# Kernel optimization log

Hardware: AMD Instinct MI355X
Metric: run time of the kernel (lower is better)

Reference implementation:

```python
import jax, jax.numpy as jnp
from jax import lax
import numpy as np

B, L, H, P, M = 8, 4096, 256, 512, 1024  # batch, seq_len, h_dim, ssm state dim (2*h), mlp hidden (4*h)

def _ln(x):
    m = jnp.mean(x, -1, keepdims=True)
    v = jnp.mean((x - m) ** 2, -1, keepdims=True)
    return (x - m) * lax.rsqrt(v + 1e-6)

def _mod(x, shift, scale):
    return x * (1.0 + scale[:, None, :]) + shift[:, None, :]

def _mlp(x, w1, b1, w2, b2):
    h = jax.nn.gelu(x @ w1.T + b1, approximate=False)
    return h @ w2.T + b2

def _s5(u, Lre, Lim, Bre, Bim, Cre, Cim, D, log_step):
    # Diagonal S5 with ZOH discretization and bidirectional parallel associative scan.
    Lam = Lre + 1j * Lim                                     # [P] complex diagonal A
    dt = jnp.exp(log_step)                                   # [P]
    Lbar = jnp.exp(Lam * dt)                                 # [P]
    Bbar = ((Lbar - 1.0) / Lam)[:, None] * (Bre + 1j * Bim)  # [P,H]
    Bu = jnp.einsum('blh,ph->blp', u + 0j, Bbar)             # [B,L,P] complex
    a = jnp.broadcast_to(Lbar, Bu.shape)
    def comb(e1, e2):
        a1, b1 = e1
        a2, b2 = e2
        return a2 * a1, a2 * b1 + b2
    xs_f = lax.associative_scan(comb, (a, Bu), axis=1)[1]
    xs_b = lax.associative_scan(comb, (a, Bu[:, ::-1]), axis=1)[1][:, ::-1]
    xs = jnp.concatenate([xs_f, xs_b], axis=-1)              # [B,L,2P]
    y = 2.0 * jnp.real(jnp.einsum('blp,hp->blh', xs, Cre + 1j * Cim))
    return y + D * u

def setup_inputs() -> dict:
    key = jax.random.key(0)
    kit = iter(jax.random.split(key, 80))
    def nrm(shape, s=1.0):
        return jax.random.normal(next(kit), shape, dtype=jnp.float32) * s
    d = {}
    d['ppg_signal'] = nrm((B, H, L))
    d['x_t'] = nrm((B, H, L))
    d['cond'] = nrm((B, H))
    d['w_ada'] = nrm((12 * H, H), 0.02)
    d['b_ada'] = jnp.zeros((12 * H,), jnp.float32)
    for pfx in ('ppg', 'tgt'):
        d[pfx + '_Lre'] = -0.5 - jax.random.uniform(next(kit), (P,), dtype=jnp.float32)
        d[pfx + '_Lim'] = jnp.pi * jnp.arange(P, dtype=jnp.float32)
        d[pfx + '_Bre'] = nrm((P, H), 1.0 / np.sqrt(H))
        d[pfx + '_Bim'] = nrm((P, H), 1.0 / np.sqrt(H))
        d[pfx + '_Cre'] = nrm((H, 2 * P), 1.0 / np.sqrt(2 * P))
        d[pfx + '_Cim'] = nrm((H, 2 * P), 1.0 / np.sqrt(2 * P))
        d[pfx + '_D'] = nrm((H,))
        d[pfx + '_log_step'] = jnp.log(0.001) + (jnp.log(0.1) - jnp.log(0.001)) * jax.random.uniform(next(kit), (P,), dtype=jnp.float32)
    for pfx in ('pre_ppg', 'mlp_ppg', 'pre_tgt', 'post_tgt', 'mlp_tgt'):
        d[pfx + '_w1'] = nrm((M, H), 0.02)
        d[pfx + '_b1'] = jnp.zeros((M,), jnp.float32)
        d[pfx + '_w2'] = nrm((H, M), 0.02)
        d[pfx + '_b2'] = jnp.zeros((H,), jnp.float32)
    return d

def reference(ppg_signal, x_t, cond, w_ada, b_ada, ppg_Lre, ppg_Lim, ppg_Bre, ppg_Bim, ppg_Cre, ppg_Cim, ppg_D, ppg_log_step, tgt_Lre, tgt_Lim, tgt_Bre, tgt_Bim, tgt_Cre, tgt_Cim, tgt_D, tgt_log_step, pre_ppg_w1, pre_ppg_b1, pre_ppg_w2, pre_ppg_b2, mlp_ppg_w1, mlp_ppg_b1, mlp_ppg_w2, mlp_ppg_b2, pre_tgt_w1, pre_tgt_b1, pre_tgt_w2, pre_tgt_b2, post_tgt_w1, post_tgt_b1, post_tgt_w2, post_tgt_b2, mlp_tgt_w1, mlp_tgt_b1, mlp_tgt_w2, mlp_tgt_b2):
    p = jnp.swapaxes(ppg_signal, 1, 2)  # [B,L,H]
    t = jnp.swapaxes(x_t, 1, 2)         # [B,L,H]
    mods = jnp.split(jax.nn.silu(cond) @ w_ada.T + b_ada, 12, axis=1)
    (sh_sp, sc_sp, g_sp, sh_mp, sc_mp, g_mp, sh_st, sc_st, g_st, sh_mt, sc_mt, g_mt) = mods
    res_p = p
    ppg_cond = g_sp[:, None, :] * _s5(_mod(_ln(p), sh_sp, sc_sp), ppg_Lre, ppg_Lim, ppg_Bre, ppg_Bim, ppg_Cre, ppg_Cim, ppg_D, ppg_log_step)
    p = res_p + ppg_cond
    p = res_p + g_mp[:, None, :] * _mlp(_mod(_ln(p), sh_mp, sc_mp), mlp_ppg_w1, mlp_ppg_b1, mlp_ppg_w2, mlp_ppg_b2)
    res_t = t
    tc = g_st[:, None, :] * _s5(_mod(_ln(t), sh_st, sc_st), tgt_Lre, tgt_Lim, tgt_Bre, tgt_Bim, tgt_Cre, tgt_Cim, tgt_D, tgt_log_step)
    pc = _mlp(ppg_cond, pre_ppg_w1, pre_ppg_b1, pre_ppg_w2, pre_ppg_b2)
    tc = _mlp(tc, pre_tgt_w1, pre_tgt_b1, pre_tgt_w2, pre_tgt_b2) + pc
    tc = _mlp(tc, post_tgt_w1, post_tgt_b1, post_tgt_w2, post_tgt_b2)
    t2 = res_t + tc
    dx = res_t + g_mt[:, None, :] * _mlp(_mod(_ln(t2), sh_mt, sc_mt), mlp_tgt_w1, mlp_tgt_b1, mlp_tgt_w2, mlp_tgt_b2)
    return jnp.swapaxes(p, 1, 2), jnp.swapaxes(dx, 1, 2)
```

## Files before the change

kernel.cpp:

```cpp
#include <hip/hip_runtime.h>
#include <hip/hip_bf16.h>
#include <math.h>

typedef unsigned short u16;
typedef unsigned int   u32;
typedef __bf16 bf16x8 __attribute__((ext_vector_type(8)));
typedef u16    u16x8  __attribute__((ext_vector_type(8)));
typedef float  f32x4  __attribute__((ext_vector_type(4)));

#define B_  8
#define L_  4096
#define H_  256
#define P_  512
#define NC_ 32
#define CH_ 128

__device__ __forceinline__ float bf2f(u16 v) { return __uint_as_float(((u32)v) << 16); }
__device__ __forceinline__ u16 f2bf(float f) {
  u32 u = __float_as_uint(f);
  u32 r = u + 0x7FFFu + ((u >> 16) & 1u);
  return (u16)(r >> 16);
}

__device__ __forceinline__ void gload16(const u16* g, u16* l) {
  __builtin_amdgcn_global_load_lds((const __attribute__((address_space(1))) u32*)g,
                                   (__attribute__((address_space(3))) u32*)l, 16, 0, 0);
}

struct F2B10 { const float* s[10]; };
__global__ __launch_bounds__(256) void k_f2b10(F2B10 a, u16* __restrict__ dst) {
  int g = blockIdx.y;
  int i = (blockIdx.x << 8) + threadIdx.x;
  dst[(size_t)g * 262144 + i] = f2bf(a.s[g][i]);
}

__global__ __launch_bounds__(256) void k_mods(const float* __restrict__ cond,
                                              const float* __restrict__ wada,
                                              const float* __restrict__ bada,
                                              float* __restrict__ mods) {
  __shared__ float s[256];
  int b = blockIdx.y;
  int j = (blockIdx.x << 8) + threadIdx.x;
  float c = cond[b * 256 + threadIdx.x];
  s[threadIdx.x] = c / (1.0f + expf(-c));
  __syncthreads();
  float acc = bada[j];
  const float* wr = wada + (size_t)j * 256;
#pragma unroll 8
  for (int k = 0; k < 256; ++k) acc += s[k] * wr[k];
  mods[b * 3072 + j] = acc;
}

__global__ __launch_bounds__(256) void k_tin2(const float* __restrict__ inP,
                                              const float* __restrict__ inT,
                                              u16* __restrict__ Pt, u16* __restrict__ Tt,
                                              int b0, int nb) {
  __shared__ u16 tile[64][65];
  int z = blockIdx.z;
  int sel = (z >= nb);
  int b = sel ? z - nb : z;
  const float* in = sel ? inT : inP;
  u16* out = sel ? Tt : Pt;
  int l0 = blockIdx.x << 6, h0 = blockIdx.y << 6;
  int tx = threadIdx.x, ty = threadIdx.y;
#pragma unroll
  for (int i = 0; i < 16; ++i) {
    int h = h0 + ty + i * 4;
    tile[ty + i * 4][tx] = f2bf(in[((size_t)(b0 + b) * 256 + h) * 4096 + l0 + tx]);
  }
  __syncthreads();
#pragma unroll
  for (int i = 0; i < 16; ++i) {
    int l = l0 + ty + i * 4;
    out[((size_t)b * 4096 + l) * 256 + h0 + tx] = tile[tx][ty + i * 4];
  }
}
__global__ __launch_bounds__(256) void k_tout(const u16* __restrict__ src, float* __restrict__ dst) {
  __shared__ u16 tile[64][65];
  int b = blockIdx.z, l0 = blockIdx.x << 6, h0 = blockIdx.y << 6;
  int tx = threadIdx.x, ty = threadIdx.y;
#pragma unroll
  for (int i = 0; i < 16; ++i) {
    int l = l0 + ty + i * 4;
    tile[ty + i * 4][tx] = src[((size_t)b * 4096 + l) * 256 + h0 + tx];
  }
  __syncthreads();
#pragma unroll
  for (int i = 0; i < 16; ++i) {
    int h = h0 + ty + i * 4;
    dst[((size_t)b * 256 + h) * 4096 + l0 + tx] = bf2f(tile[tx][ty + i * 4]);
  }
}

__global__ __launch_bounds__(256) void k_lnmod(const u16* __restrict__ X, u16* __restrict__ U,
                                               const float* __restrict__ mods,
                                               int sh_off, int sc_off, int b0) {
  int t = blockIdx.x, tid = threadIdx.x;
  int b = b0 + (t >> 12);
  float x = bf2f(X[(size_t)t * 256 + tid]);
  float s1 = x, s2 = x * x;
#pragma unroll
  for (int off = 32; off; off >>= 1) { s1 += __shfl_xor(s1, off); s2 += __shfl_xor(s2, off); }
  __shared__ float red[8];
  int w = tid >> 6;
  if ((tid & 63) == 0) { red[w * 2] = s1; red[w * 2 + 1] = s2; }
  __syncthreads();
  s1 = red[0] + red[2] + red[4] + red[6];
  s2 = red[1] + red[3] + red[5] + red[7];
  float m = s1 * (1.0f / 256.0f);
  float v = fmaxf(s2 * (1.0f / 256.0f) - m * m, 0.0f);
  float r = rsqrtf(v + 1e-6f);
  float sc = mods[b * 3072 + sc_off + tid];
  float sh = mods[b * 3072 + sh_off + tid];
  U[(size_t)t * 256 + tid] = f2bf((x - m) * r * (1.0f + sc) + sh);
}

__global__ __launch_bounds__(256) void k_wb2(const float* Lre0, const float* Lim0, const float* ls0,
                                             const float* Bre0, const float* Bim0, u16* WB0,
                                             const float* Lre1, const float* Lim1, const float* ls1,
                                             const float* Bre1, const float* Bim1, u16* WB1) {
  int s = blockIdx.y;
  const float* Lre = s ? Lre1 : Lre0;
  const float* Lim = s ? Lim1 : Lim0;
  const float* ls  = s ? ls1  : ls0;
  const float* Bre = s ? Bre1 : Bre0;
  const float* Bim = s ? Bim1 : Bim0;
  u16* WB = s ? WB1 : WB0;
  int p = blockIdx.x, h = threadIdx.x;
  float lre = Lre[p], lim = Lim[p];
  float dt = expf(ls[p]);
  float er = expf(lre * dt), sn, cs;
  sincosf(lim * dt, &sn, &cs);
  float ar = er * cs - 1.0f, ai = er * sn;
  float den = lre * lre + lim * lim;
  float cr = (ar * lre + ai * lim) / den;
  float ci = (ai * lre - ar * lim) / den;
  float br = Bre[p * 256 + h], bi = Bim[p * 256 + h];
  WB[(size_t)(2 * p) * 256 + h]     = f2bf(cr * br - ci * bi);
  WB[(size_t)(2 * p + 1) * 256 + h] = f2bf(cr * bi + ci * br);
}

__global__ __launch_bounds__(256) void k_wc2(const float* Cre0, const float* Cim0, u16* W0,
                                             const float* Cre1, const float* Cim1, u16* W1) {
  int s = blockIdx.y;
  const float* Cre = s ? Cre1 : Cre0;
  const float* Cim = s ? Cim1 : Cim0;
  u16* W = s ? W1 : W0;
  int idx = (blockIdx.x << 8) + threadIdx.x;
  int h = idx >> 11, k = idx & 2047;
  int sc = ((k >> 10) << 9) + ((k & 1023) >> 1);
  float v = (k & 1) ? -2.0f * Cim[h * 1024 + sc] : 2.0f * Cre[h * 1024 + sc];
  W[idx] = f2bf(v);
}

__device__ __forceinline__ float2 lbar_of(const float* Lre, const float* Lim, const float* lstep,
                                          int p, float mul) {
  float dt = expf(lstep[p]) * mul;
  float er = expf(Lre[p] * dt), sn, cs;
  sincosf(Lim[p] * dt, &sn, &cs);
  return make_float2(er * cs, er * sn);
}

__global__ __launch_bounds__(256) void k_scanA2(const float* Lre, const float* Lim, const float* lstep,
                                                const u16* __restrict__ Bu,
                                                float2* __restrict__ car_f, float2* __restrict__ car_b) {
  int g = (blockIdx.x << 8) + threadIdx.x;
  int p = g & 511, rb = (g >> 9) & 31, bl = g >> 14;
  float2 a = lbar_of(Lre, Lim, lstep, p, 1.0f);
  float fr = 0.f, fi = 0.f;
  float br_ = 0.f, bi_ = 0.f;
  float pr = 1.f, pi = 0.f;
  const u32* bup = (const u32*)Bu + (((size_t)((bl << 12) + rb * CH_)) << 9) + p;
#pragma unroll 4
  for (int j = 0; j < CH_; ++j) {
    u32 w = *bup;
    float er = bf2f((u16)(w & 0xFFFF)), ei = bf2f((u16)(w >> 16));
    float nr = a.x * fr - a.y * fi + er;
    float ni = a.x * fi + a.y * fr + ei;
    fr = nr; fi = ni;
    br_ += pr * er - pi * ei;
    bi_ += pr * ei + pi * er;
    float npr = pr * a.x - pi * a.y;
    float npi = pr * a.y + pi * a.x;
    pr = npr; pi = npi;
    bup += 512;
  }
  car_f[g] = make_float2(fr, fi);
  car_b[((size_t)bl << 14) + ((size_t)(31 - rb) << 9) + p] = make_float2(br_, bi_);
}

__global__ __launch_bounds__(256) void k_scanB2(const float* Lre, const float* Lim, const float* lstep,
                                                const float2* __restrict__ car_f,
                                                const float2* __restrict__ car_b,
                                                float2* __restrict__ cin_f, float2* __restrict__ cin_b) {
  int dir = blockIdx.y;
  int g = (blockIdx.x << 8) + threadIdx.x;
  int p = g & 511, bl = g >> 9;
  float2 an = lbar_of(Lre, Lim, lstep, p, (float)CH_);
  const float2* car = dir ? car_b : car_f;
  float2* cin = dir ? cin_b : cin_f;
  float xr = 0.f, xi = 0.f;
  size_t base = (size_t)bl * 16384 + p;
  for (int c = 0; c < NC_; ++c) {
    size_t src = base + (size_t)c * 512;
    size_t dst = dir ? (base + (size_t)(31 - c) * 512) : src;
    cin[dst] = make_float2(xr, xi);
    float2 E = car[src];
    float nr = an.x * xr - an.y * xi + E.x;
    float ni = an.x * xi + an.y * xr + E.y;
    xr = nr; xi = ni;
  }
}

__global__ __launch_bounds__(256) void k_scanC2(const float* Lre, const float* Lim, const float* lstep,
                                                u16* __restrict__ Bu,
                                                const float2* __restrict__ cin_f,
                                                const float2* __restrict__ cin_b,
                                                u32* __restrict__ xsf) {
  int g = (blockIdx.x << 8) + threadIdx.x;
  int p = g & 511, rb = (g >> 9) & 31, bl = g >> 14;
  float2 a = lbar_of(Lre, Lim, lstep, p, 1.0f);
  size_t rowbase = (((size_t)((bl << 12) + rb * CH_)) << 9) + p;
  const u32* bup = (const u32*)Bu + rowbase;
  u32* xop = xsf + rowbase;
  float2 c0 = cin_f[g];
  float xr = c0.x, xi = c0.y;
#pragma unroll 4
  for (int j = 0; j < CH_; ++j) {
    u32 w = *bup;
    float er = bf2f((u16)(w & 0xFFFF)), ei = bf2f((u16)(w >> 16));
    float nr = a.x * xr - a.y * xi + er;
    float ni = a.x * xi + a.y * xr + ei;
    xr = nr; xi = ni;
    *xop = (u32)f2bf(xr) | ((u32)f2bf(xi) << 16);
    bup += 512; xop += 512;
  }
  u32* bwp = (u32*)Bu + rowbase + ((size_t)(CH_ - 1) << 9);
  c0 = cin_b[g];
  xr = c0.x; xi = c0.y;
#pragma unroll 4
  for (int j = 0; j < CH_; ++j) {
    u32 w = *bwp;
    float er = bf2f((u16)(w & 0xFFFF)), ei = bf2f((u16)(w >> 16));
    float nr = a.x * xr - a.y * xi + er;
    float ni = a.x * xi + a.y * xr + ei;
    xr = nr; xi = ni;
    *bwp = (u32)f2bf(xr) | ((u32)f2bf(xi) << 16);
    bwp -= 512;
  }
}

template <int MODE>
__global__ __launch_bounds__(256, 8) void gemm64s_bt(const u16* __restrict__ A, const u16* __restrict__ A2,
                                                     const u16* __restrict__ W, u16* __restrict__ out,
                                                     int M, int N, int K,
                                                     const float* __restrict__ bias,
                                                     const float* __restrict__ gmods, int g_off, int b0,
                                                     const u16* __restrict__ res, const u16* __restrict__ add,
                                                     const u16* __restrict__ uin, const float* __restrict__ Dv,
                                                     u16* __restrict__ out2) {
  __shared__ __align__(16) u16 sA[64 * 64];
  __shared__ __align__(16) u16 sB[64 * 64];
  const int tid = threadIdx.x;
  const int wave = tid >> 6, lane = tid & 63;

  const int nx = gridDim.x;
  const int tot = nx * gridDim.y;
  const int bid = blockIdx.x + nx * blockIdx.y;
  const int wid = (bid & 7) * (tot >> 3) + (bid >> 3);
  const int nxs = 31 - __clz(nx);
  const int m0 = (wid >> nxs) << 6;
  const int n0 = (wid & (nx - 1)) << 6;

  const int wm = (wave >> 1) << 5, wn = (wave & 1) << 5;
  const int lr = lane & 15;
  const int lk = (lane >> 4) << 3;
  const int swz = (lr & 7) << 3;

  f32x4 acc[2][2];
#pragma unroll
  for (int i = 0; i < 2; ++i)
#pragma unroll
    for (int j = 0; j < 2; ++j) acc[i][j] = (f32x4){0.f, 0.f, 0.f, 0.f};

  const int As = (MODE == 6) ? 1024 : K;
  const int gr = lane >> 3;
  const int gc = ((lane & 7) ^ gr) << 3;
  const u16* Ag  = A + (size_t)(m0 + wave * 16 + gr) * As + gc;
  const u16* A2g = (MODE == 6) ? (A2 + (size_t)(m0 + wave * 16 + gr) * 1024 + gc) : nullptr;
  const u16* Wg  = W + (size_t)(n0 + wave * 16 + gr) * K + gc;
  u16* lA = &sA[(wave * 16) * 64];
  u16* lB = &sB[(wave * 16) * 64];

  for (int k0 = 0; k0 < K; k0 += 64) {
    const u16* Asrc = (MODE == 6 && k0 >= 1024) ? (A2g + (k0 - 1024)) : (Ag + k0);
    __syncthreads();
    gload16(Asrc, lA);
    gload16(Asrc + (size_t)8 * As, lA + 8 * 64);
    gload16(Wg + k0, lB);
    gload16(Wg + (size_t)8 * K + k0, lB + 8 * 64);
    __syncthreads();
#pragma unroll
    for (int kk = 0; kk < 64; kk += 32) {
      bf16x8 af[2], bfr[2];
#pragma unroll
      for (int i = 0; i < 2; ++i)
        af[i] = *(const bf16x8*)&sA[(wm + i * 16 + lr) * 64 + ((kk + lk) ^ swz)];
#pragma unroll
      for (int j = 0; j < 2; ++j)
        bfr[j] = *(const bf16x8*)&sB[(wn + j * 16 + lr) * 64 + ((kk + lk) ^ swz)];
#pragma unroll
      for (int i = 0; i < 2; ++i)
#pragma unroll
        for (int j = 0; j < 2; ++j)
          acc[i][j] = __builtin_amdgcn_mfma_f32_16x16x32_bf16(af[i], bfr[j], acc[i][j], 0, 0, 0);
    }
  }

  const int lq = lane >> 4;
#pragma unroll
  for (int i = 0; i < 2; ++i)
#pragma unroll
    for (int j = 0; j < 2; ++j)
#pragma unroll
      for (int r = 0; r < 4; ++r) {
        int m = m0 + wm + i * 16 + lq * 4 + r;
        int n = n0 + wn + j * 16 + lr;
        float v = acc[i][j][r];
        size_t o = (size_t)m * N + n;
        if (MODE == 0) {
          out[o] = f2bf(v);
        } else if (MODE == 1) {
          float z = v + bias[n];
          out[o] = f2bf(0.5f * z * (1.0f + erff(z * 0.70710678118f)));
        } else if (MODE == 2) {
          out[o] = f2bf(v + bias[n]);
        } else if (MODE == 3) {
          out[o] = f2bf(v + bias[n] + bf2f(add[o]));
        } else if (MODE == 4) {
          out[o] = f2bf(v + bias[n] + bf2f(res[o]));
        } else if (MODE == 5) {
          int bb = b0 + (m >> 12);
          float g = gmods[bb * 3072 + g_off + n];
          out[o] = f2bf(bf2f(res[o]) + g * (v + bias[n]));
        } else {
          int bb = b0 + (m >> 12);
          float g = gmods[bb * 3072 + g_off + n];
          float c1 = g * (v + Dv[n] * bf2f(uin[o]));
          out[o] = f2bf(c1);
          if (out2) out2[o] = f2bf(bf2f(res[o]) + c1);
        }
      }
}

extern "C" void kernel_launch(void* const* d_in, const int* in_sizes, int n_in,
                              void* d_out, int out_size, void* d_ws, size_t ws_size,
                              hipStream_t stream) {
  (void)in_sizes; (void)n_in; (void)out_size;
  float* outp = (float*)d_out;
#define F(i) ((const float*)d_in[i])

  char* ws = (char*)d_ws;
  float*  mods  = (float*)(ws + 0x000000);
  u16*    WBp   = (u16*)(ws + 0x020000);
  u16*    WBt   = (u16*)(ws + 0x0A0000);
  u16*    WCp2  = (u16*)(ws + 0x120000);
  u16*    WCt2  = (u16*)(ws + 0x220000);
  float2* car_f = (float2*)(ws + 0x320000);
  float2* car_b = (float2*)(ws + 0x420000);
  float2* cin_f = (float2*)(ws + 0x520000);
  float2* cin_b = (float2*)(ws + 0x620000);
  u16*    wcv   = (u16*)(ws + 0x720000);

  const int widx[10] = {21, 23, 25, 27, 29, 31, 33, 35, 37, 39};
  const u16* WV[41];
  F2B10 fb;
  for (int i = 0; i < 10; ++i) {
    fb.s[i] = F(widx[i]);
    WV[widx[i]] = wcv + (size_t)i * 262144;
  }
  k_f2b10<<<dim3(1024, 10), 256, 0, stream>>>(fb, wcv);

  int nb = 1;
  for (int cand = 8; cand >= 1; cand >>= 1) {
    size_t need = (size_t)0x1000000 + (size_t)cand * 4096 * 8192;
    if (need <= ws_size) { nb = cand; break; }
  }
  const int R = nb * 4096;
  char* big = ws + 0x1000000;
  size_t sb = (size_t)R * 512;
  u16* Pt   = (u16*)(big);
  u16* Tt   = (u16*)(big + sb);
  u16* u_   = (u16*)(big + 2 * sb);
  u16* pcnd = (u16*)(big + 3 * sb);
  u16* p1   = (u16*)(big + 4 * sb);
  u16* tcb  = (u16*)(big + 5 * sb);
  u16* tmp1 = (u16*)(big + 6 * sb);
  u16* tmp2 = (u16*)(big + 7 * sb);
  u16* Bu   = (u16*)(big + 8 * sb);
  u16* xsf  = (u16*)(big + 12 * sb);

  k_mods<<<dim3(12, 8), 256, 0, stream>>>(F(2), F(3), F(4), mods);
  k_wb2<<<dim3(512, 2), 256, 0, stream>>>(F(5), F(6), F(12), F(7), F(8), WBp,
                                          F(13), F(14), F(20), F(15), F(16), WBt);
  k_wc2<<<dim3(2048, 2), 256, 0, stream>>>(F(9), F(10), WCp2, F(17), F(18), WCt2);

  for (int b0 = 0; b0 < 8; b0 += nb) {
#define GEMM(MODE, Aa, Ww, Oo, Nn, Kk, biasp, goff, resp, addp)                                    \
  gemm64s_bt<MODE><<<dim3((Nn) / 64, R / 64), 256, 0, stream>>>(                                   \
      (const u16*)(Aa), nullptr, (const u16*)(Ww), (u16*)(Oo), R, (Nn), (Kk),                      \
      (const float*)(biasp), mods, (goff), b0, (const u16*)(resp), (const u16*)(addp),             \
      nullptr, nullptr, nullptr)
#define SCANS2(Lr, Li, Ls)                                                                         \
  do {                                                                                             \
    k_scanA2<<<nb * 64, 256, 0, stream>>>(Lr, Li, Ls, Bu, car_f, car_b);                           \
    k_scanB2<<<dim3(nb * 2, 2), 256, 0, stream>>>(Lr, Li, Ls, car_f, car_b, cin_f, cin_b);         \
    k_scanC2<<<nb * 64, 256, 0, stream>>>(Lr, Li, Ls, Bu, cin_f, cin_b, (u32*)xsf);                \
  } while (0)
#define CAT(Ww, Oo, goff, resp, uinp, Dp, o2)                                                      \
  gemm64s_bt<6><<<dim3(4, R / 64), 256, 0, stream>>>(                                              \
      (const u16*)xsf, (const u16*)Bu, (const u16*)(Ww), (u16*)(Oo), R, 256, 2048, nullptr, mods,  \
      (goff), b0, (const u16*)(resp), nullptr, (const u16*)(uinp), (const float*)(Dp), (u16*)(o2))

    k_tin2<<<dim3(64, 4, 2 * nb), dim3(64, 4), 0, stream>>>(F(0), F(1), Pt, Tt, b0, nb);

    k_lnmod<<<R, 256, 0, stream>>>(Pt, u_, mods, 0 * 256, 1 * 256, b0);
    GEMM(0, u_, WBp, Bu, 1024, 256, nullptr, 0, nullptr, nullptr);
    SCANS2(F(5), F(6), F(12));
    CAT(WCp2, pcnd, 2 * 256, Pt, u_, F(11), p1);

    k_lnmod<<<R, 256, 0, stream>>>(p1, tmp1, mods, 3 * 256, 4 * 256, b0);
    GEMM(1, tmp1, WV[25], Bu, 1024, 256, F(26), 0, nullptr, nullptr);
    GEMM(5, Bu, WV[27], tmp2, 256, 1024, F(28), 5 * 256, Pt, nullptr);
    k_tout<<<dim3(64, 4, nb), dim3(64, 4), 0, stream>>>(tmp2, outp + (size_t)b0 * 1048576);

    k_lnmod<<<R, 256, 0, stream>>>(Tt, u_, mods, 6 * 256, 7 * 256, b0);
    GEMM(0, u_, WBt, Bu, 1024, 256, nullptr, 0, nullptr, nullptr);
    SCANS2(F(13), F(14), F(20));
    CAT(WCt2, tcb, 8 * 256, nullptr, u_, F(19), nullptr);

    GEMM(1, pcnd, WV[21], Bu, 1024, 256, F(22), 0, nullptr, nullptr);
    GEMM(2, Bu, WV[23], tmp1, 256, 1024, F(24), 0, nullptr, nullptr);
    GEMM(1, tcb, WV[29], Bu, 1024, 256, F(30), 0, nullptr, nullptr);
    GEMM(3, Bu, WV[31], tmp2, 256, 1024, F(32), 0, nullptr, tmp1);
    GEMM(1, tmp2, WV[33], Bu, 1024, 256, F(34), 0, nullptr, nullptr);
    GEMM(4, Bu, WV[35], tcb, 256, 1024, F(36), 0, Tt, nullptr);
    k_lnmod<<<R, 256, 0, stream>>>(tcb, tmp1, mods, 9 * 256, 10 * 256, b0);
    GEMM(1, tmp1, WV[37], Bu, 1024, 256, F(38), 0, nullptr, nullptr);
    GEMM(5, Bu, WV[39], tmp2, 256, 1024, F(40), 11 * 256, Tt, nullptr);
    k_tout<<<dim3(64, 4, nb), dim3(64, 4), 0, stream>>>(tmp2, outp + 8388608 + (size_t)b0 * 1048576);

#undef GEMM
#undef SCANS2
#undef CAT
  }
#undef F
}
```

Baseline: 1.085 ms.

## Fuse output transpose into GEMM epilogue, merge pre-MLP GEMMs, drop scan carry pass

Three fusions. The separate output transpose kernels are removed: a new GEMM epilogue mode stages gated residual results in shared memory and writes fp32 directly in [B,H,L] layout. The two pre-MLP first-layer GEMMs become one launch over stacked rows, selecting weights by row half. Their second layers become one K=2048 GEMM over concatenated weights, which sums pc and tc without an intermediate buffer. The middle scan-carry kernel is also eliminated; each chunk thread recomputes its incoming carry serially from the chunk carries, trading redundant work for fewer launches and less memory traffic.

Result: no change. 1.096 ms (+1.0%).

```diff
diff --git a/kernel.cpp b/kernel.cpp
--- a/kernel.cpp
+++ b/kernel.cpp
@@ -32,6 +32,15 @@
   int g = blockIdx.y;
   int i = (blockIdx.x << 8) + threadIdx.x;
   dst[(size_t)g * 262144 + i] = f2bf(a.s[g][i]);
+}
+
+__global__ __launch_bounds__(256) void k_wcat(const float* __restrict__ Wa,
+                                              const float* __restrict__ Wb,
+                                              u16* __restrict__ Wc) {
+  int idx = (blockIdx.x << 8) + threadIdx.x;
+  int n = idx >> 11, k = idx & 2047;
+  float v = (k < 1024) ? Wa[n * 1024 + k] : Wb[n * 1024 + (k - 1024)];
+  Wc[idx] = f2bf(v);
 }
 
 __global__ __launch_bounds__(256) void k_mods(const float* __restrict__ cond,
@@ -73,22 +82,6 @@
   for (int i = 0; i < 16; ++i) {
     int l = l0 + ty + i * 4;
     out[((size_t)b * 4096 + l) * 256 + h0 + tx] = tile[tx][ty + i * 4];
-  }
-}
-__global__ __launch_bounds__(256) void k_tout(const u16* __restrict__ src, float* __restrict__ dst) {
-  __shared__ u16 tile[64][65];
-  int b = blockIdx.z, l0 = blockIdx.x << 6, h0 = blockIdx.y << 6;
-  int tx = threadIdx.x, ty = threadIdx.y;
-#pragma unroll
-  for (int i = 0; i < 16; ++i) {
-    int l = l0 + ty + i * 4;
-    tile[ty + i * 4][tx] = src[((size_t)b * 4096 + l) * 256 + h0 + tx];
-  }
-  __syncthreads();
-#pragma unroll
-  for (int i = 0; i < 16; ++i) {
-    int h = h0 + ty + i * 4;
-    dst[((size_t)b * 256 + h) * 4096 + l0 + tx] = bf2f(tile[tx][ty + i * 4]);
   }
 }
 
@@ -189,42 +182,26 @@
   car_b[((size_t)bl << 14) + ((size_t)(31 - rb) << 9) + p] = make_float2(br_, bi_);
 }
 
-__global__ __launch_bounds__(256) void k_scanB2(const float* Lre, const float* Lim, const float* lstep,
+__global__ __launch_bounds__(256) void k_scanC2(const float* Lre, const float* Lim, const float* lstep,
+                                                u16* __restrict__ Bu,
                                                 const float2* __restrict__ car_f,
                                                 const float2* __restrict__ car_b,
-                                                float2* __restrict__ cin_f, float2* __restrict__ cin_b) {
-  int dir = blockIdx.y;
-  int g = (blockIdx.x << 8) + threadIdx.x;
-  int p = g & 511, bl = g >> 9;
-  float2 an = lbar_of(Lre, Lim, lstep, p, (float)CH_);
-  const float2* car = dir ? car_b : car_f;
-  float2* cin = dir ? cin_b : cin_f;
-  float xr = 0.f, xi = 0.f;
-  size_t base = (size_t)bl * 16384 + p;
-  for (int c = 0; c < NC_; ++c) {
-    size_t src = base + (size_t)c * 512;
-    size_t dst = dir ? (base + (size_t)(31 - c) * 512) : src;
-    cin[dst] = make_float2(xr, xi);
-    float2 E = car[src];
-    float nr = an.x * xr - an.y * xi + E.x;
-    float ni = an.x * xi + an.y * xr + E.y;
-    xr = nr; xi = ni;
-  }
-}
-
-__global__ __launch_bounds__(256) void k_scanC2(const float* Lre, const float* Lim, const float* lstep,
-                                                u16* __restrict__ Bu,
-                                                const float2* __restrict__ cin_f,
-                                                const float2* __restrict__ cin_b,
                                                 u32* __restrict__ xsf) {
   int g = (blockIdx.x << 8) + threadIdx.x;
   int p = g & 511, rb = (g >> 9) & 31, bl = g >> 14;
   float2 a = lbar_of(Lre, Lim, lstep, p, 1.0f);
+  float2 an = lbar_of(Lre, Lim, lstep, p, (float)CH_);
+  size_t cbase = ((size_t)bl << 14) + p;
+  float xr = 0.f, xi = 0.f;
+  for (int c = 0; c < rb; ++c) {
+    float2 E = car_f[cbase + ((size_t)c << 9)];
+    float nr = an.x * xr - an.y * xi + E.x;
+    float ni = an.x * xi + an.y * xr + E.y;
+    xr = nr; xi = ni;
+  }
   size_t rowbase = (((size_t)((bl << 12) + rb * CH_)) << 9) + p;
   const u32* bup = (const u32*)Bu + rowbase;
   u32* xop = xsf + rowbase;
-  float2 c0 = cin_f[g];
-  float xr = c0.x, xi = c0.y;
 #pragma unroll 4
   for (int j = 0; j < CH_; ++j) {
     u32 w = *bup;
@@ -235,9 +212,15 @@
     *xop = (u32)f2bf(xr) | ((u32)f2bf(xi) << 16);
     bup += 512; xop += 512;
   }
+  xr = 0.f; xi = 0.f;
+  int nn = 31 - rb;
+  for (int c = 0; c < nn; ++c) {
+    float2 E = car_b[cbase + ((size_t)c << 9)];
+    float nr = an.x * xr - an.y * xi + E.x;
+    float ni = an.x * xi + an.y * xr + E.y;
+    xr = nr; xi = ni;
+  }
   u32* bwp = (u32*)Bu + rowbase + ((size_t)(CH_ - 1) << 9);
-  c0 = cin_b[g];
-  xr = c0.x; xi = c0.y;
 #pragma unroll 4
   for (int j = 0; j < CH_; ++j) {
     u32 w = *bwp;
@@ -251,16 +234,19 @@
 }
 
 template <int MODE>
-__global__ __launch_bounds__(256, 8) void gemm64s_bt(const u16* __restrict__ A, const u16* __restrict__ A2,
-                                                     const u16* __restrict__ W, u16* __restrict__ out,
-                                                     int M, int N, int K,
-                                                     const float* __restrict__ bias,
-                                                     const float* __restrict__ gmods, int g_off, int b0,
-                                                     const u16* __restrict__ res, const u16* __restrict__ add,
-                                                     const u16* __restrict__ uin, const float* __restrict__ Dv,
-                                                     u16* __restrict__ out2) {
-  __shared__ __align__(16) u16 sA[64 * 64];
-  __shared__ __align__(16) u16 sB[64 * 64];
+__global__ __launch_bounds__(256, 8) void gemm64s_bt(
+    const u16* __restrict__ A, const u16* __restrict__ A2,
+    const u16* __restrict__ W, const u16* __restrict__ W2,
+    u16* __restrict__ out, float* __restrict__ fdst,
+    int N, int K, int halfM,
+    const float* __restrict__ bias, const float* __restrict__ bias2,
+    const float* __restrict__ gmods, int g_off, int b0,
+    const u16* __restrict__ res, const u16* __restrict__ uin,
+    const float* __restrict__ Dv, u16* __restrict__ out2) {
+  constexpr int SMW = (MODE == 7) ? 8704 : 8192;
+  __shared__ __align__(16) u16 smem[SMW];
+  u16* sA = smem;
+  u16* sB = smem + 4096;
   const int tid = threadIdx.x;
   const int wave = tid >> 6, lane = tid & 63;
 
@@ -283,17 +269,21 @@
 #pragma unroll
     for (int j = 0; j < 2; ++j) acc[i][j] = (f32x4){0.f, 0.f, 0.f, 0.f};
 
-  const int As = (MODE == 6) ? 1024 : K;
+  const bool hi = (W2 != nullptr) && (m0 >= halfM);
+  const u16* Wuse = hi ? W2 : W;
+  const float* buse = hi ? bias2 : bias;
+
+  const int As = A2 ? 1024 : K;
   const int gr = lane >> 3;
   const int gc = ((lane & 7) ^ gr) << 3;
   const u16* Ag  = A + (size_t)(m0 + wave * 16 + gr) * As + gc;
-  const u16* A2g = (MODE == 6) ? (A2 + (size_t)(m0 + wave * 16 + gr) * 1024 + gc) : nullptr;
-  const u16* Wg  = W + (size_t)(n0 + wave * 16 + gr) * K + gc;
+  const u16* A2g = A2 ? (A2 + (size_t)(m0 + wave * 16 + gr) * 1024 + gc) : nullptr;
+  const u16* Wg  = Wuse + (size_t)(n0 + wave * 16 + gr) * K + gc;
   u16* lA = &sA[(wave * 16) * 64];
   u16* lB = &sB[(wave * 16) * 64];
 
   for (int k0 = 0; k0 < K; k0 += 64) {
-    const u16* Asrc = (MODE == 6 && k0 >= 1024) ? (A2g + (k0 - 1024)) : (Ag + k0);
+    const u16* Asrc = (A2 && k0 >= 1024) ? (A2g + (k0 - 1024)) : (Ag + k0);
     __syncthreads();
     gload16(Asrc, lA);
     gload16(Asrc + (size_t)8 * As, lA + 8 * 64);
@@ -318,6 +308,35 @@
   }
 
   const int lq = lane >> 4;
+  if (MODE == 7) {
+    float* lf = (float*)smem;
+    __syncthreads();
+#pragma unroll
+    for (int i = 0; i < 2; ++i)
+#pragma unroll
+      for (int j = 0; j < 2; ++j)
+#pragma unroll
+        for (int r = 0; r < 4; ++r) {
+          int ml = wm + i * 16 + lq * 4 + r;
+          int nl = wn + j * 16 + lr;
+          int m = m0 + ml, n = n0 + nl;
+          int bb = b0 + (m >> 12);
+          float g = gmods[bb * 3072 + g_off + n];
+          size_t o = (size_t)m * N + n;
+          lf[nl * 68 + ml] = bf2f(res[o]) + g * (acc[i][j][r] + bias[n]);
+        }
+    __syncthreads();
+    int row = tid >> 2;
+    int mb  = (tid & 3) << 4;
+    int b   = b0 + (m0 >> 12);
+    int l   = (m0 & 4095) + mb;
+    float* dp = fdst + ((size_t)b * 256 + (n0 + row)) * 4096 + l;
+    const float* sp = lf + row * 68 + mb;
+#pragma unroll
+    for (int q = 0; q < 16; q += 4) *(f32x4*)(dp + q) = *(const f32x4*)(sp + q);
+    return;
+  }
+
 #pragma unroll
   for (int i = 0; i < 2; ++i)
 #pragma unroll
@@ -331,18 +350,12 @@
         if (MODE == 0) {
           out[o] = f2bf(v);
         } else if (MODE == 1) {
-          float z = v + bias[n];
+          float z = v + buse[n];
           out[o] = f2bf(0.5f * z * (1.0f + erff(z * 0.70710678118f)));
-        } else if (MODE == 2) {
-          out[o] = f2bf(v + bias[n]);
-        } else if (MODE == 3) {
-          out[o] = f2bf(v + bias[n] + bf2f(add[o]));
         } else if (MODE == 4) {
           out[o] = f2bf(v + bias[n] + bf2f(res[o]));
-        } else if (MODE == 5) {
-          int bb = b0 + (m >> 12);
-          float g = gmods[bb * 3072 + g_off + n];
-          out[o] = f2bf(bf2f(res[o]) + g * (v + bias[n]));
+        } else if (MODE == 8) {
+          out[o] = f2bf(v + bias[n] + bias2[n]);
         } else {
           int bb = b0 + (m >> 12);
           float g = gmods[bb * 3072 + g_off + n];
@@ -366,11 +379,10 @@
   u16*    WBt   = (u16*)(ws + 0x0A0000);
   u16*    WCp2  = (u16*)(ws + 0x120000);
   u16*    WCt2  = (u16*)(ws + 0x220000);
-  float2* car_f = (float2*)(ws + 0x320000);
-  float2* car_b = (float2*)(ws + 0x420000);
-  float2* cin_f = (float2*)(ws + 0x520000);
-  float2* cin_b = (float2*)(ws + 0x620000);
-  u16*    wcv   = (u16*)(ws + 0x720000);
+  u16*    Wcat  = (u16*)(ws + 0x320000);
+  float2* car_f = (float2*)(ws + 0x420000);
+  float2* car_b = (float2*)(ws + 0x520000);
+  u16*    wcv   = (u16*)(ws + 0x620000);
 
   const int widx[10] = {21, 23, 25, 27, 29, 31, 33, 35, 37, 39};
   const u16* WV[41];
@@ -380,6 +392,7 @@
     WV[widx[i]] = wcv + (size_t)i * 262144;
   }
   k_f2b10<<<dim3(1024, 10), 256, 0, stream>>>(fb, wcv);
+  k_wcat<<<2048, 256, 0, stream>>>(F(23), F(31), Wcat);
 
   int nb = 1;
   for (int cand = 8; cand >= 1; cand >>= 1) {
@@ -393,8 +406,8 @@
   u16* Tt   = (u16*)(big + sb);
   u16* u_   = (u16*)(big + 2 * sb);
   u16* pcnd = (u16*)(big + 3 * sb);
-  u16* p1   = (u16*)(big + 4 * sb);
-  u16* tcb  = (u16*)(big + 5 * sb);
+  u16* tcb  = (u16*)(big + 4 * sb);
+  u16* p1   = (u16*)(big + 5 * sb);
   u16* tmp1 = (u16*)(big + 6 * sb);
   u16* tmp2 = (u16*)(big + 7 * sb);
   u16* Bu   = (u16*)(big + 8 * sb);
@@ -406,53 +419,43 @@
   k_wc2<<<dim3(2048, 2), 256, 0, stream>>>(F(9), F(10), WCp2, F(17), F(18), WCt2);
 
   for (int b0 = 0; b0 < 8; b0 += nb) {
-#define GEMM(MODE, Aa, Ww, Oo, Nn, Kk, biasp, goff, resp, addp)                                    \
-  gemm64s_bt<MODE><<<dim3((Nn) / 64, R / 64), 256, 0, stream>>>(                                   \
-      (const u16*)(Aa), nullptr, (const u16*)(Ww), (u16*)(Oo), R, (Nn), (Kk),                      \
-      (const float*)(biasp), mods, (goff), b0, (const u16*)(resp), (const u16*)(addp),             \
-      nullptr, nullptr, nullptr)
+#define G64(MODE, Aa, A2a, Ww, W2w, Oo, Fd, Nn, Kk, hM, B1, B2, GOFF, RESP, UINP, DVP, O2, NX, NY) \
+  gemm64s_bt<MODE><<<dim3(NX, NY), 256, 0, stream>>>(                                              \
+      (const u16*)(Aa), (const u16*)(A2a), (const u16*)(Ww), (const u16*)(W2w), (u16*)(Oo),        \
+      (float*)(Fd), (Nn), (Kk), (hM), (const float*)(B1), (const float*)(B2), mods, (GOFF), b0,    \
+      (const u16*)(RESP), (const u16*)(UINP), (const float*)(DVP), (u16*)(O2))
 #define SCANS2(Lr, Li, Ls)                                                                         \
   do {                                                                                             \
     k_scanA2<<<nb * 64, 256, 0, stream>>>(Lr, Li, Ls, Bu, car_f, car_b);                           \
-    k_scanB2<<<dim3(nb * 2, 2), 256, 0, stream>>>(Lr, Li, Ls, car_f, car_b, cin_f, cin_b);         \
-    k_scanC2<<<nb * 64, 256, 0, stream>>>(Lr, Li, Ls, Bu, cin_f, cin_b, (u32*)xsf);                \
+    k_scanC2<<<nb * 64, 256, 0, stream>>>(Lr, Li, Ls, Bu, car_f, car_b, (u32*)xsf);                \
   } while (0)
-#define CAT(Ww, Oo, goff, resp, uinp, Dp, o2)                                                      \
-  gemm64s_bt<6><<<dim3(4, R / 64), 256, 0, stream>>>(                                              \
-      (const u16*)xsf, (const u16*)Bu, (const u16*)(Ww), (u16*)(Oo), R, 256, 2048, nullptr, mods,  \
-      (goff), b0, (const u16*)(resp), nullptr, (const u16*)(uinp), (const float*)(Dp), (u16*)(o2))
 
     k_tin2<<<dim3(64, 4, 2 * nb), dim3(64, 4), 0, stream>>>(F(0), F(1), Pt, Tt, b0, nb);
 
     k_lnmod<<<R, 256, 0, stream>>>(Pt, u_, mods, 0 * 256, 1 * 256, b0);
-    GEMM(0, u_, WBp, Bu, 1024, 256, nullptr, 0, nullptr, nullptr);
+    G64(0, u_, 0, WBp, 0, Bu, 0, 1024, 256, 0, 0, 0, 0, 0, 0, 0, 0, 16, R / 64);
     SCANS2(F(5), F(6), F(12));
-    CAT(WCp2, pcnd, 2 * 256, Pt, u_, F(11), p1);
+    G64(6, xsf, Bu, WCp2, 0, pcnd, 0, 256, 2048, 0, 0, 0, 2 * 256, Pt, u_, F(11), p1, 4, R / 64);
 
     k_lnmod<<<R, 256, 0, stream>>>(p1, tmp1, mods, 3 * 256, 4 * 256, b0);
-    GEMM(1, tmp1, WV[25], Bu, 1024, 256, F(26), 0, nullptr, nullptr);
-    GEMM(5, Bu, WV[27], tmp2, 256, 1024, F(28), 5 * 256, Pt, nullptr);
-    k_tout<<<dim3(64, 4, nb), dim3(64, 4), 0, stream>>>(tmp2, outp + (size_t)b0 * 1048576);
+    G64(1, tmp1, 0, WV[25], 0, Bu, 0, 1024, 256, 0, F(26), 0, 0, 0, 0, 0, 0, 16, R / 64);
+    G64(7, Bu, 0, WV[27], 0, 0, outp, 256, 1024, 0, F(28), 0, 5 * 256, Pt, 0, 0, 0, 4, R / 64);
 
     k_lnmod<<<R, 256, 0, stream>>>(Tt, u_, mods, 6 * 256, 7 * 256, b0);
-    GEMM(0, u_, WBt, Bu, 1024, 256, nullptr, 0, nullptr, nullptr);
+    G64(0, u_, 0, WBt, 0, Bu, 0, 1024, 256, 0, 0, 0, 0, 0, 0, 0, 0, 16, R / 64);
     SCANS2(F(13), F(14), F(20));
-    CAT(WCt2, tcb, 8 * 256, nullptr, u_, F(19), nullptr);
-
-    GEMM(1, pcnd, WV[21], Bu, 1024, 256, F(22), 0, nullptr, nullptr);
-    GEMM(2, Bu, WV[23], tmp1, 256, 1024, F(24), 0, nullptr, nullptr);
-    GEMM(1, tcb, WV[29], Bu, 1024, 256, F(30), 0, nullptr, nullptr);
-    GEMM(3, Bu, WV[31], tmp2, 256, 1024, F(32), 0, nullptr, tmp1);
-    GEMM(1, tmp2, WV[33], Bu, 1024, 256, F(34), 0, nullptr, nullptr);
-    GEMM(4, Bu, WV[35], tcb, 256, 1024, F(36), 0, Tt, nullptr);
+    G64(6, xsf, Bu, WCt2, 0, tcb, 0, 256, 2048, 0, 0, 0, 8 * 256, 0, u_, F(19), 0, 4, R / 64);
+
+    G64(1, pcnd, 0, WV[21], WV[29], Bu, 0, 1024, 256, R, F(22), F(30), 0, 0, 0, 0, 0, 16, 2 * R / 64);
+    G64(8, Bu, Bu + (size_t)R * 1024, Wcat, 0, tmp2, 0, 256, 2048, 0, F(24), F(32), 0, 0, 0, 0, 0, 4, R / 64);
+    G64(1, tmp2, 0, WV[33], 0, Bu, 0, 1024, 256, 0, F(34), 0, 0, 0, 0, 0, 0, 16, R / 64);
+    G64(4, Bu, 0, WV[35], 0, tcb, 0, 256, 1024, 0, F(36), 0, 0, Tt, 0, 0, 0, 4, R / 64);
     k_lnmod<<<R, 256, 0, stream>>>(tcb, tmp1, mods, 9 * 256, 10 * 256, b0);
-    GEMM(1, tmp1, WV[37], Bu, 1024, 256, F(38), 0, nullptr, nullptr);
-    GEMM(5, Bu, WV[39], tmp2, 256, 1024, F(40), 11 * 256, Tt, nullptr);
-    k_tout<<<dim3(64, 4, nb), dim3(64, 4), 0, stream>>>(tmp2, outp + 8388608 + (size_t)b0 * 1048576);
-
-#undef GEMM
+    G64(1, tmp1, 0, WV[37], 0, Bu, 0, 1024, 256, 0, F(38), 0, 0, 0, 0, 0, 0, 16, R / 64);
+    G64(7, Bu, 0, WV[39], 0, 0, outp + 8388608, 256, 1024, 0, F(40), 0, 11 * 256, Tt, 0, 0, 0, 4, R / 64);
+
+#undef G64
 #undef SCANS2
-#undef CAT
   }
 #undef F
 }
```
